# Optimization experiments

Measured on AMD Instinct MI355X. Metric: run time of the kernel, lower is better.

## Reference

```python
import jax, jax.numpy as jnp
import numpy as np

N = 10000; E = 160000; NF = 5; EF = 3; H = 8; C = 128; HC = H * C; G = 16

def _glorot(key, shape):
    s = float(np.sqrt(6.0 / (shape[0] + shape[-1])))
    return jax.random.uniform(key, shape, minval=-s, maxval=s, dtype=jnp.float32)

def setup_inputs():
    key = jax.random.key(0)
    ks = jax.random.split(key, 32)
    inp = {}
    inp["x"] = jax.random.normal(ks[0], (N, NF), dtype=jnp.float32)
    inp["edge_index"] = jax.random.randint(ks[1], (2, E), 0, N, dtype=jnp.int32)
    inp["edge_attr"] = jax.random.normal(ks[2], (E, EF), dtype=jnp.float32)
    inp["batch"] = jnp.sort(jax.random.randint(ks[3], (N,), 0, G, dtype=jnp.int32))
    ins = [NF, HC, HC, HC]
    i = 4
    for l in range(4):
        inp[f"W{l+1}"] = _glorot(ks[i], (ins[l], HC)); i += 1
        inp[f"We{l+1}"] = _glorot(ks[i], (EF, HC)); i += 1
        inp[f"as{l+1}"] = _glorot(ks[i], (H, C)); i += 1
        inp[f"ad{l+1}"] = _glorot(ks[i], (H, C)); i += 1
        inp[f"ae{l+1}"] = _glorot(ks[i], (H, C)); i += 1
        inp[f"b{l+1}"] = jnp.zeros((HC if l < 3 else C,), jnp.float32)
    inp["lin_w"] = _glorot(ks[i], (C, 1)) * 2.0
    inp["lin_b"] = jnp.zeros((1,), jnp.float32)
    return inp

def _gat(x, src, dst, ea, W, We, a_s, a_d, a_e, bias, concat):
    # PyG GATConv with edge_dim, add_self_loops=True, fill_value='mean'
    n = x.shape[0]
    cnt = jax.ops.segment_sum(jnp.ones((src.shape[0],), x.dtype), dst, n)
    loop_attr = jax.ops.segment_sum(ea, dst, n) / jnp.maximum(cnt, 1.0)[:, None]
    sl = jnp.arange(n, dtype=src.dtype)
    src2 = jnp.concatenate([src, sl])
    dst2 = jnp.concatenate([dst, sl])
    ea2 = jnp.concatenate([ea, loop_attr], axis=0)
    xl = (x @ W).reshape(n, H, C)                       # [N,H,C]
    a_src = jnp.einsum("nhc,hc->nh", xl, a_s)
    a_dst = jnp.einsum("nhc,hc->nh", xl, a_d)
    el = (ea2 @ We).reshape(-1, H, C)                    # [E2,H,C]
    alpha = a_src[src2] + a_dst[dst2] + jnp.einsum("ehc,hc->eh", el, a_e)
    alpha = jax.nn.leaky_relu(alpha, 0.2)
    m = jax.ops.segment_max(alpha, dst2, n)
    m = jnp.where(jnp.isfinite(m), m, 0.0)
    ex = jnp.exp(alpha - m[dst2])
    den = jax.ops.segment_sum(ex, dst2, n)
    alpha = ex / (den[dst2] + 1e-16)                     # segment softmax over dst
    out = jax.ops.segment_sum(alpha[:, :, None] * xl[src2], dst2, n)  # [N,H,C]
    if concat:
        return out.reshape(n, HC) + bias
    return out.mean(axis=1) + bias

def reference(x, edge_index, edge_attr, batch,
              W1, We1, as1, ad1, ae1, b1,
              W2, We2, as2, ad2, ae2, b2,
              W3, We3, as3, ad3, ae3, b3,
              W4, We4, as4, ad4, ae4, b4,
              lin_w, lin_b):
    src, dst = edge_index[0], edge_index[1]
    h = jax.nn.elu(_gat(x, src, dst, edge_attr, W1, We1, as1, ad1, ae1, b1, True))
    h = jax.nn.elu(_gat(h, src, dst, edge_attr, W2, We2, as2, ad2, ae2, b2, True))
    h = jax.nn.elu(_gat(h, src, dst, edge_attr, W3, We3, as3, ad3, ae3, b3, True))
    h = jax.nn.elu(_gat(h, src, dst, edge_attr, W4, We4, as4, ad4, ae4, b4, False))
    cnt = jax.ops.segment_sum(jnp.ones((N,), h.dtype), batch, G)
    pooled = jax.ops.segment_sum(h, batch, G) / jnp.maximum(cnt, 1.0)[:, None]
    return (pooled @ lin_w + lin_b).squeeze(-1)
```

## Files before the change

kernel.cpp:

```cpp
#include <hip/hip_runtime.h>
#include <math.h>

#define Nn 10000
#define En 160000
#define NF 5
#define EF 3
#define Hh 8
#define Cc 128
#define HC 1024
#define Gg 16

#define Mpad 10112

typedef __attribute__((ext_vector_type(8))) _Float16 half8;
typedef __attribute__((ext_vector_type(4))) float f32x4;


__device__ __forceinline__ void gl_lds16(const void* g, void* l) {
    __builtin_amdgcn_global_load_lds((const __attribute__((address_space(1))) void*)g,
                                     (__attribute__((address_space(3))) void*)l, 16, 0, 0);
}

__device__ __forceinline__ float elu_f(float v) {
    return (v > 0.f) ? v : expm1f(v);
}


__global__ void deg_sum_k(const int* __restrict__ dst, const float* __restrict__ ea,
                          int* __restrict__ cnt, float* __restrict__ sum_ea) {
    int e = blockIdx.x * 256 + threadIdx.x;
    if (e >= En) return;
    int d = dst[e];
    atomicAdd(&cnt[d], 1);
    atomicAdd(&sum_ea[d * 3 + 0], ea[e * 3 + 0]);
    atomicAdd(&sum_ea[d * 3 + 1], ea[e * 3 + 1]);
    atomicAdd(&sum_ea[d * 3 + 2], ea[e * 3 + 2]);
}

__global__ void finish_loop_k(const int* __restrict__ cnt, float* __restrict__ loop_attr) {
    int n = blockIdx.x * 256 + threadIdx.x;
    if (n >= Nn) return;
    float s = 1.0f / fmaxf((float)cnt[n], 1.0f);
    loop_attr[n * 3 + 0] *= s;
    loop_attr[n * 3 + 1] *= s;
    loop_attr[n * 3 + 2] *= s;
}

__global__ __launch_bounds__(1024) void scan_k(const int* __restrict__ cnt,
                                               int* __restrict__ rowptr,
                                               int* __restrict__ fillptr) {
    __shared__ int sh[1024];
    int tid = threadIdx.x;
    int base = 0;
    for (int chunk = 0; chunk < Nn; chunk += 1024) {
        int i = chunk + tid;
        int v = (i < Nn) ? cnt[i] : 0;
        sh[tid] = v;
        __syncthreads();
        for (int off = 1; off < 1024; off <<= 1) {
            int t = (tid >= off) ? sh[tid - off] : 0;
            __syncthreads();
            sh[tid] += t;
            __syncthreads();
        }
        int excl = sh[tid] - v;
        if (i < Nn) { rowptr[i] = base + excl; fillptr[i] = base + excl; }
        int total = sh[1023];
        __syncthreads();
        base += total;
    }
    if (tid == 0) rowptr[Nn] = base;
}

__global__ void csr_fill_k(const int* __restrict__ src, const int* __restrict__ dst,
                           const float* __restrict__ ea, int* __restrict__ fillptr,
                           int* __restrict__ srcP, float4* __restrict__ eaP) {
    int e = blockIdx.x * 256 + threadIdx.x;
    if (e >= En) return;
    int d = dst[e];
    int pos = atomicAdd(&fillptr[d], 1);
    srcP[pos] = src[e];
    eaP[pos] = make_float4(ea[e * 3 + 0], ea[e * 3 + 1], ea[e * 3 + 2], 0.f);
}

__global__ void bounds_k(const int* __restrict__ batch, int* __restrict__ gstart) {
    int i = blockIdx.x * 256 + threadIdx.x;
    if (i >= Nn) return;
    int b = batch[i];
    if (i == 0) {
        for (int g = 0; g <= b; ++g) gstart[g] = 0;
    } else {
        int pb = batch[i - 1];
        for (int g = pb + 1; g <= b; ++g) gstart[g] = i;
    }
    if (i == Nn - 1) {
        for (int g = b + 1; g <= Gg; ++g) gstart[g] = Nn;
    }
}


__global__ void wae_all_k(const float* __restrict__ We1, const float* __restrict__ ae1,
                          const float* __restrict__ We2, const float* __restrict__ ae2,
                          const float* __restrict__ We3, const float* __restrict__ ae3,
                          const float* __restrict__ We4, const float* __restrict__ ae4,
                          float* __restrict__ w_ae_all) {
    int t = threadIdx.x;
    if (t >= 96) return;
    int l = t / 24, idx = t % 24;
    int f = idx >> 3, h = idx & 7;
    const float* We = (l == 0) ? We1 : (l == 1) ? We2 : (l == 2) ? We3 : We4;
    const float* ae = (l == 0) ? ae1 : (l == 1) ? ae2 : (l == 2) ? ae3 : ae4;
    float s = 0.f;
    for (int c = 0; c < Cc; ++c) s += We[f * HC + h * Cc + c] * ae[h * Cc + c];
    w_ae_all[l * 24 + f * 8 + h] = s;
}

__global__ __launch_bounds__(1024) void wsplit_all_k(const float* __restrict__ W2,
                                                     const float* __restrict__ W3,
                                                     const float* __restrict__ W4,
                                                     _Float16* __restrict__ Wt16) {
    __shared__ float tile[32][33];
    int z = blockIdx.z;
    const float* W = (z == 0) ? W2 : (z == 1) ? W3 : W4;
    int nb = blockIdx.x * 32, kb = blockIdx.y * 32;
    tile[threadIdx.y][threadIdx.x] = W[(size_t)(kb + threadIdx.y) * HC + nb + threadIdx.x];
    __syncthreads();
    float x = tile[threadIdx.x][threadIdx.y];
    int n = nb + threadIdx.y, k = kb + threadIdx.x;
    Wt16[(size_t)z * HC * HC + (size_t)n * HC + k] = (_Float16)x;
}


__global__ void gemm_k5(const float* __restrict__ x, const float* __restrict__ Wm,
                        const float* __restrict__ a_s, const float* __restrict__ a_d,
                        _Float16* __restrict__ out16,
                        float* __restrict__ a_srcB, float* __restrict__ a_dstB) {
    int n = blockIdx.x;
    int tid = threadIdx.x;
    __shared__ float xr[8];
    __shared__ float vrow[HC];
    if (tid < NF) xr[tid] = x[n * NF + tid];
    __syncthreads();
    float x0 = xr[0], x1 = xr[1], x2 = xr[2], x3 = xr[3], x4 = xr[4];
    for (int j = tid; j < HC; j += 256) {
        float v = x0 * Wm[j] + x1 * Wm[HC + j] + x2 * Wm[2 * HC + j]
                + x3 * Wm[3 * HC + j] + x4 * Wm[4 * HC + j];
        out16[(size_t)n * HC + j] = (_Float16)v;
        vrow[j] = v;
    }
    __syncthreads();
    int w = tid >> 6, lane = tid & 63;
#pragma unroll
    for (int q = 0; q < 2; ++q) {
        int h = w * 2 + q;
        float v0 = vrow[h * Cc + lane], v1 = vrow[h * Cc + 64 + lane];
        float s1 = v0 * a_s[h * Cc + lane] + v1 * a_s[h * Cc + 64 + lane];
        float s2 = v0 * a_d[h * Cc + lane] + v1 * a_d[h * Cc + 64 + lane];
#pragma unroll
        for (int off = 32; off; off >>= 1) {
            s1 += __shfl_xor(s1, off);
            s2 += __shfl_xor(s2, off);
        }
        if (lane == 0) { a_srcB[n * 8 + h] = s1; a_dstB[n * 8 + h] = s2; }
    }
}

__global__ __launch_bounds__(256) void gemm_mfma(const _Float16* __restrict__ A,
                                                 const _Float16* __restrict__ Bt,
                                                 const float* __restrict__ a_s,
                                                 const float* __restrict__ a_d,
                                                 _Float16* __restrict__ C16,
                                                 float* __restrict__ a_srcB,
                                                 float* __restrict__ a_dstB) {
    __shared__ _Float16 As[128 * 32];
    __shared__ _Float16 Bs[128 * 32];
    __shared__ float ps[128][2];
    __shared__ float pd[128][2];
    int tid = threadIdx.x;
    int wave = tid >> 6, lane = tid & 63;
    int wr = wave >> 1, wc = wave & 1;
    int row0 = blockIdx.y * 128;
    int col0 = blockIdx.x * 128;
    int h = blockIdx.x;

    f32x4 acc[4][4];
#pragma unroll
    for (int i = 0; i < 4; ++i)
#pragma unroll
        for (int j = 0; j < 4; ++j) acc[i][j] = (f32x4){0.f, 0.f, 0.f, 0.f};

    int srow = lane >> 2;
    int scol = (lane & 3) * 8;
    int fr = lane & 15;
    int fk = (lane >> 4) * 8;

    for (int kb = 0; kb < 1024; kb += 32) {
#pragma unroll
        for (int cc = 0; cc < 2; ++cc) {
            int c = wave + cc * 4;
            int r = c * 16 + srow;
            gl_lds16(A + (size_t)(row0 + r) * 1024 + kb + scol, &As[c * 512 + lane * 8]);
            gl_lds16(Bt + (size_t)(col0 + r) * 1024 + kb + scol, &Bs[c * 512 + lane * 8]);
        }
        __syncthreads();

        half8 af[4], bf[4];
#pragma unroll
        for (int i = 0; i < 4; ++i)
            af[i] = *(const half8*)&As[(wr * 64 + i * 16 + fr) * 32 + fk];
#pragma unroll
        for (int j = 0; j < 4; ++j)
            bf[j] = *(const half8*)&Bs[(wc * 64 + j * 16 + fr) * 32 + fk];
#pragma unroll
        for (int i = 0; i < 4; ++i)
#pragma unroll
            for (int j = 0; j < 4; ++j)
                acc[i][j] = __builtin_amdgcn_mfma_f32_16x16x32_f16(af[i], bf[j], acc[i][j],
                                                                   0, 0, 0);
        __syncthreads();
    }

    int cn = lane & 15, rq = (lane >> 4) * 4;
#pragma unroll
    for (int i = 0; i < 4; ++i) {
        int rbase = row0 + wr * 64 + i * 16 + rq;
#pragma unroll
        for (int j = 0; j < 4; ++j) {
            int col = col0 + wc * 64 + j * 16 + cn;
#pragma unroll
            for (int r = 0; r < 4; ++r) {
                int row = rbase + r;
                if (row < Nn) C16[(size_t)row * HC + col] = (_Float16)acc[i][j][r];
            }
        }
    }
    float asv[4], adv[4];
#pragma unroll
    for (int j = 0; j < 4; ++j) {
        int c = wc * 64 + j * 16 + cn;
        asv[j] = a_s[h * Cc + c];
        adv[j] = a_d[h * Cc + c];
    }
#pragma unroll
    for (int i = 0; i < 4; ++i)
#pragma unroll
        for (int r = 0; r < 4; ++r) {
            float rs = acc[i][0][r] * asv[0] + acc[i][1][r] * asv[1]
                     + acc[i][2][r] * asv[2] + acc[i][3][r] * asv[3];
            float rd = acc[i][0][r] * adv[0] + acc[i][1][r] * adv[1]
                     + acc[i][2][r] * adv[2] + acc[i][3][r] * adv[3];
#pragma unroll
            for (int off = 1; off < 16; off <<= 1) {
                rs += __shfl_xor(rs, off);
                rd += __shfl_xor(rd, off);
            }
            if (cn == 0) {
                int rib = wr * 64 + i * 16 + rq + r;
                ps[rib][wc] = rs;
                pd[rib][wc] = rd;
            }
        }
    __syncthreads();
    if (tid < 128) {
        int row = row0 + tid;
        if (row < Nn) {
            a_srcB[row * 8 + h] = ps[tid][0] + ps[tid][1];
            a_dstB[row * 8 + h] = pd[tid][0] + pd[tid][1];
        }
    }
}


__global__ __launch_bounds__(256) void aggregate_k(const _Float16* __restrict__ xl16,
                                                   const float4* __restrict__ eaP,
                                                   const float* __restrict__ loop_attr,
                                                   const float* __restrict__ a_srcB,
                                                   const float* __restrict__ a_dstB,
                                                   const float* __restrict__ w_ae,
                                                   const int* __restrict__ rowptr,
                                                   const int* __restrict__ srcP,
                                                   const float* __restrict__ bias,
                                                   const float* __restrict__ lin_w,
                                                   _Float16* __restrict__ A2,
                                                   float* __restrict__ dnode,
                                                   int raw_mode) {
    int n = (blockIdx.x * 256 + threadIdx.x) >> 6;
    int lane = threadIdx.x & 63;
    if (n >= Nn) return;
    int beg = rowptr[n], end = rowptr[n + 1];
    int hh = lane & 7;
    int slot = lane >> 3;
    int hc = lane >> 3;

    float w0 = w_ae[hh], w1 = w_ae[8 + hh], w2 = w_ae[16 + hh];
    float adst_n = a_dstB[n * 8 + hh];
    float asrc_n = a_srcB[n * 8 + hh];
    float f0 = loop_attr[n * 3 + 0], f1 = loop_attr[n * 3 + 1], f2 = loop_attr[n * 3 + 2];
    float av = asrc_n + adst_n + f0 * w0 + f1 * w1 + f2 * w2;
    float aself = (av > 0.f) ? av : 0.2f * av;

    float m = (slot == 0) ? aself : -3.0e38f;
    float s = (slot == 0) ? 1.0f : 0.0f;
    for (int i = beg + slot; i < end; i += 8) {
        int sn = srcP[i];
        float4 e4 = eaP[i];
        float a = a_srcB[sn * 8 + hh] + adst_n + e4.x * w0 + e4.y * w1 + e4.z * w2;
        a = (a > 0.f) ? a : 0.2f * a;
        if (a > m) { s = s * __expf(m - a) + 1.0f; m = a; }
        else s += __expf(a - m);
    }
#pragma unroll
    for (int off = 8; off < 64; off <<= 1) {
        float mo = __shfl_xor(m, off);
        float so = __shfl_xor(s, off);
        float M = fmaxf(m, mo);
        s = s * __expf(m - M) + so * __expf(mo - M);
        m = M;
    }
    float inv = 1.f / (s + 1e-16f);
    float wself = __expf(aself - m) * inv;

    float m_c = __shfl(m, hc);
    float inv_c = __shfl(inv, hc);
    float wself_c = __shfl(wself, hc);
    float adst_nc = __shfl(adst_n, hc);
    float w0c = w_ae[hc], w1c = w_ae[8 + hc], w2c = w_ae[16 + hc];

    float acc[16];
    {
        const _Float16* r = xl16 + (size_t)n * HC + lane * 16;
        half8 r0 = *(const half8*)r;
        half8 r1 = *(const half8*)(r + 8);
#pragma unroll
        for (int j = 0; j < 8; ++j) {
            acc[j] = wself_c * (float)r0[j];
            acc[8 + j] = wself_c * (float)r1[j];
        }
    }
    int loff = lane * 16;
    for (int i0 = beg; i0 < end; i0 += 4) {
        int last = end - 1;
        bool v1 = (i0 + 1 < end), v2 = (i0 + 2 < end), v3 = (i0 + 3 < end);
        int i1 = v1 ? i0 + 1 : last;
        int i2 = v2 ? i0 + 2 : last;
        int i3 = v3 ? i0 + 3 : last;
        int s0 = srcP[i0], s1 = srcP[i1], s2 = srcP[i2], s3 = srcP[i3];
        float4 e0 = eaP[i0], e1 = eaP[i1], e2 = eaP[i2], e3 = eaP[i3];
        float as0 = a_srcB[s0 * 8 + hc], as1 = a_srcB[s1 * 8 + hc];
        float as2 = a_srcB[s2 * 8 + hc], as3 = a_srcB[s3 * 8 + hc];
        const _Float16* p0 = xl16 + (size_t)s0 * HC + loff;
        const _Float16* p1 = xl16 + (size_t)s1 * HC + loff;
        const _Float16* p2 = xl16 + (size_t)s2 * HC + loff;
        const _Float16* p3 = xl16 + (size_t)s3 * HC + loff;
        half8 q0a = *(const half8*)p0, q0b = *(const half8*)(p0 + 8);
        half8 q1a = *(const half8*)p1, q1b = *(const half8*)(p1 + 8);
        half8 q2a = *(const half8*)p2, q2b = *(const half8*)(p2 + 8);
        half8 q3a = *(const half8*)p3, q3b = *(const half8*)(p3 + 8);
        float al0 = as0 + adst_nc + e0.x * w0c + e0.y * w1c + e0.z * w2c;
        float al1 = as1 + adst_nc + e1.x * w0c + e1.y * w1c + e1.z * w2c;
        float al2 = as2 + adst_nc + e2.x * w0c + e2.y * w1c + e2.z * w2c;
        float al3 = as3 + adst_nc + e3.x * w0c + e3.y * w1c + e3.z * w2c;
        al0 = (al0 > 0.f) ? al0 : 0.2f * al0;
        al1 = v1 ? ((al1 > 0.f) ? al1 : 0.2f * al1) : -3.0e38f;
        al2 = v2 ? ((al2 > 0.f) ? al2 : 0.2f * al2) : -3.0e38f;
        al3 = v3 ? ((al3 > 0.f) ? al3 : 0.2f * al3) : -3.0e38f;
        float u0 = __expf(al0 - m_c) * inv_c;
        float u1 = __expf(al1 - m_c) * inv_c;
        float u2 = __expf(al2 - m_c) * inv_c;
        float u3 = __expf(al3 - m_c) * inv_c;
#pragma unroll
        for (int j = 0; j < 8; ++j) {
            float t0 = acc[j], t1 = acc[8 + j];
            t0 = fmaf(u0, (float)q0a[j], t0);  t1 = fmaf(u0, (float)q0b[j], t1);
            t0 = fmaf(u1, (float)q1a[j], t0);  t1 = fmaf(u1, (float)q1b[j], t1);
            t0 = fmaf(u2, (float)q2a[j], t0);  t1 = fmaf(u2, (float)q2b[j], t1);
            t0 = fmaf(u3, (float)q3a[j], t0);  t1 = fmaf(u3, (float)q3b[j], t1);
            acc[j] = t0; acc[8 + j] = t1;
        }
    }

    if (!raw_mode) {
        int ch = lane * 16;
        half8 hv0, hv1;
#pragma unroll
        for (int j = 0; j < 8; ++j) {
            hv0[j] = (_Float16)elu_f(acc[j] + bias[ch + j]);
            hv1[j] = (_Float16)elu_f(acc[8 + j] + bias[ch + 8 + j]);
        }
        _Float16* p = A2 + (size_t)n * 1024 + ch;
        *(half8*)p = hv0;
        *(half8*)(p + 8) = hv1;
    } else {
#pragma unroll
        for (int off = 8; off < 64; off <<= 1)
#pragma unroll
            for (int j = 0; j < 16; ++j) acc[j] += __shfl_xor(acc[j], off);
        int c0 = (lane & 7) * 16;
        float partial = 0.f;
#pragma unroll
        for (int j = 0; j < 16; ++j) {
            float v = elu_f(acc[j] * 0.125f + bias[c0 + j]);
            partial = fmaf(v, lin_w[c0 + j], partial);
        }
#pragma unroll
        for (int off = 1; off < 8; off <<= 1) partial += __shfl_xor(partial, off);
        if (lane == 0) dnode[n] = partial;
    }
}


__global__ __launch_bounds__(256) void pool_final_k(const float* __restrict__ dnode,
                                                    const int* __restrict__ gstart,
                                                    const float* __restrict__ lin_b,
                                                    float* __restrict__ out) {
    __shared__ float sh[256];
    int g = blockIdx.x;
    int tid = threadIdx.x;
    int s = gstart[g], e = gstart[g + 1];
    float acc = 0.f;
    for (int n = s + tid; n < e; n += 256) acc += dnode[n];
    sh[tid] = acc;
    __syncthreads();
    for (int off = 128; off; off >>= 1) {
        if (tid < off) sh[tid] += sh[tid + off];
        __syncthreads();
    }
    if (tid == 0) out[g] = sh[0] / fmaxf((float)(e - s), 1.f) + lin_b[0];
}


extern "C" void kernel_launch(void* const* d_in, const int* in_sizes, int n_in,
                              void* d_out, int out_size, void* d_ws, size_t ws_size,
                              hipStream_t stream) {
    const float* x = (const float*)d_in[0];
    const int* ei = (const int*)d_in[1];
    const float* ea = (const float*)d_in[2];
    const int* batch = (const int*)d_in[3];
    const float *Wl[4], *Wel[4], *asl[4], *adl[4], *ael[4], *bl[4];
    for (int l = 0; l < 4; ++l) {
        Wl[l] = (const float*)d_in[4 + 6 * l];
        Wel[l] = (const float*)d_in[5 + 6 * l];
        asl[l] = (const float*)d_in[6 + 6 * l];
        adl[l] = (const float*)d_in[7 + 6 * l];
        ael[l] = (const float*)d_in[8 + 6 * l];
        bl[l] = (const float*)d_in[9 + 6 * l];
    }
    const float* lin_w = (const float*)d_in[28];
    const float* lin_b = (const float*)d_in[29];
    const int* srcA = ei;
    const int* dstA = ei + En;

    float* Wp = (float*)d_ws;
    size_t o = 0;
    _Float16* A2 = (_Float16*)(Wp + o); o += (size_t)Mpad * 512;
    _Float16* Wt16 = (_Float16*)(Wp + o); o += (size_t)3 * HC * HC / 2;
    _Float16* xl16 = (_Float16*)(Wp + o); o += (size_t)Nn * HC / 2;
    float4* eaP = (float4*)(Wp + o); o += (size_t)En * 4;
    float* loop_attr = Wp + o; o += Nn * 3;
    int* cnt = (int*)(Wp + o); o += Nn;
    int* rowptr = (int*)(Wp + o); o += Nn + 1;
    int* fillptr = (int*)(Wp + o); o += Nn;
    int* srcP = (int*)(Wp + o); o += En;
    int* gstart = (int*)(Wp + o); o += Gg + 1;
    float* a_srcB = Wp + o; o += Nn * Hh;
    float* a_dstB = Wp + o; o += Nn * Hh;
    float* w_ae_all = Wp + o; o += 128;
    float* dnode = Wp + o; o += Nn;

    hipMemsetAsync(cnt, 0, Nn * sizeof(int), stream);
    hipMemsetAsync(loop_attr, 0, Nn * 3 * sizeof(float), stream);

    deg_sum_k<<<(En + 255) / 256, 256, 0, stream>>>(dstA, ea, cnt, loop_attr);
    finish_loop_k<<<(Nn + 255) / 256, 256, 0, stream>>>(cnt, loop_attr);
    scan_k<<<1, 1024, 0, stream>>>(cnt, rowptr, fillptr);
    csr_fill_k<<<(En + 255) / 256, 256, 0, stream>>>(srcA, dstA, ea, fillptr, srcP, eaP);
    bounds_k<<<(Nn + 255) / 256, 256, 0, stream>>>(batch, gstart);
    wae_all_k<<<1, 128, 0, stream>>>(Wel[0], ael[0], Wel[1], ael[1], Wel[2], ael[2],
                                     Wel[3], ael[3], w_ae_all);
    wsplit_all_k<<<dim3(32, 32, 3), dim3(32, 32), 0, stream>>>(Wl[1], Wl[2], Wl[3], Wt16);

    for (int l = 0; l < 4; ++l) {
        if (l == 0)
            gemm_k5<<<Nn, 256, 0, stream>>>(x, Wl[0], asl[0], adl[0], xl16, a_srcB, a_dstB);
        else
            gemm_mfma<<<dim3(HC / 128, Mpad / 128), 256, 0, stream>>>(
                A2, Wt16 + (size_t)(l - 1) * HC * HC, asl[l], adl[l], xl16, a_srcB, a_dstB);
        aggregate_k<<<(Nn + 3) / 4, 256, 0, stream>>>(xl16, eaP, loop_attr, a_srcB,
                                                      a_dstB, w_ae_all + l * 24, rowptr,
                                                      srcP, bl[l], lin_w, A2, dnode,
                                                      (l == 3) ? 1 : 0);
    }
    pool_final_k<<<Gg, 256, 0, stream>>>(dnode, gstart, lin_b, (float*)d_out);
}
```

Measured before the change: 599.0 us.

## Split each node's edge aggregation across two waves and fold loop-attr normalize into scan

The aggregation kernel now gives each destination node two wavefronts that take alternating groups of edges. Their fp32 partial sums are combined through shared memory before the ELU/bias epilogue or the final-layer reduction. This raises parallelism and memory-level concurrency for the gather-bound loop, at the cost of a block barrier, an LDS round trip and duplicated softmax statistic computation. The separate loop-attribute normalization kernel is merged into the prefix-scan kernel to save one launch.

Result: no change. 603.1 us (+0.7%).

```diff
diff --git a/kernel.cpp b/kernel.cpp
--- a/kernel.cpp
+++ b/kernel.cpp
@@ -37,24 +37,22 @@
     atomicAdd(&sum_ea[d * 3 + 2], ea[e * 3 + 2]);
 }
 
-__global__ void finish_loop_k(const int* __restrict__ cnt, float* __restrict__ loop_attr) {
-    int n = blockIdx.x * 256 + threadIdx.x;
-    if (n >= Nn) return;
-    float s = 1.0f / fmaxf((float)cnt[n], 1.0f);
-    loop_attr[n * 3 + 0] *= s;
-    loop_attr[n * 3 + 1] *= s;
-    loop_attr[n * 3 + 2] *= s;
-}
-
 __global__ __launch_bounds__(1024) void scan_k(const int* __restrict__ cnt,
                                                int* __restrict__ rowptr,
-                                               int* __restrict__ fillptr) {
+                                               int* __restrict__ fillptr,
+                                               float* __restrict__ loop_attr) {
     __shared__ int sh[1024];
     int tid = threadIdx.x;
     int base = 0;
     for (int chunk = 0; chunk < Nn; chunk += 1024) {
         int i = chunk + tid;
         int v = (i < Nn) ? cnt[i] : 0;
+        if (i < Nn) {
+            float s = 1.0f / fmaxf((float)v, 1.0f);
+            loop_attr[i * 3 + 0] *= s;
+            loop_attr[i * 3 + 1] *= s;
+            loop_attr[i * 3 + 2] *= s;
+        }
         sh[tid] = v;
         __syncthreads();
         for (int off = 1; off < 1024; off <<= 1) {
@@ -284,9 +282,12 @@
                                                    _Float16* __restrict__ A2,
                                                    float* __restrict__ dnode,
                                                    int raw_mode) {
-    int n = (blockIdx.x * 256 + threadIdx.x) >> 6;
+    __shared__ float cmb[2][1024];
+    int wave = threadIdx.x >> 6;
     int lane = threadIdx.x & 63;
-    if (n >= Nn) return;
+    int nl = wave >> 1;
+    int sub = wave & 1;
+    int n = blockIdx.x * 2 + nl;
     int beg = rowptr[n], end = rowptr[n + 1];
     int hh = lane & 7;
     int slot = lane >> 3;
@@ -327,7 +328,7 @@
     float w0c = w_ae[hc], w1c = w_ae[8 + hc], w2c = w_ae[16 + hc];
 
     float acc[16];
-    {
+    if (sub == 0) {
         const _Float16* r = xl16 + (size_t)n * HC + lane * 16;
         half8 r0 = *(const half8*)r;
         half8 r1 = *(const half8*)(r + 8);
@@ -336,14 +337,17 @@
             acc[j] = wself_c * (float)r0[j];
             acc[8 + j] = wself_c * (float)r1[j];
         }
+    } else {
+#pragma unroll
+        for (int j = 0; j < 16; ++j) acc[j] = 0.f;
     }
     int loff = lane * 16;
-    for (int i0 = beg; i0 < end; i0 += 4) {
-        int last = end - 1;
-        bool v1 = (i0 + 1 < end), v2 = (i0 + 2 < end), v3 = (i0 + 3 < end);
-        int i1 = v1 ? i0 + 1 : last;
-        int i2 = v2 ? i0 + 2 : last;
-        int i3 = v3 ? i0 + 3 : last;
+    for (int i0 = beg + sub; i0 < end; i0 += 8) {
+        int i1 = i0 + 2, i2 = i0 + 4, i3 = i0 + 6;
+        bool v1 = (i1 < end), v2 = (i2 < end), v3 = (i3 < end);
+        if (!v1) i1 = i0;
+        if (!v2) i2 = i0;
+        if (!v3) i3 = i0;
         int s0 = srcP[i0], s1 = srcP[i1], s2 = srcP[i2], s3 = srcP[i3];
         float4 e0 = eaP[i0], e1 = eaP[i1], e2 = eaP[i2], e3 = eaP[i3];
         float as0 = a_srcB[s0 * 8 + hc], as1 = a_srcB[s1 * 8 + hc];
@@ -379,32 +383,48 @@
         }
     }
 
-    if (!raw_mode) {
-        int ch = lane * 16;
-        half8 hv0, hv1;
-#pragma unroll
-        for (int j = 0; j < 8; ++j) {
-            hv0[j] = (_Float16)elu_f(acc[j] + bias[ch + j]);
-            hv1[j] = (_Float16)elu_f(acc[8 + j] + bias[ch + 8 + j]);
-        }
-        _Float16* p = A2 + (size_t)n * 1024 + ch;
-        *(half8*)p = hv0;
-        *(half8*)(p + 8) = hv1;
-    } else {
-#pragma unroll
-        for (int off = 8; off < 64; off <<= 1)
-#pragma unroll
-            for (int j = 0; j < 16; ++j) acc[j] += __shfl_xor(acc[j], off);
-        int c0 = (lane & 7) * 16;
-        float partial = 0.f;
-#pragma unroll
-        for (int j = 0; j < 16; ++j) {
-            float v = elu_f(acc[j] * 0.125f + bias[c0 + j]);
-            partial = fmaf(v, lin_w[c0 + j], partial);
-        }
-#pragma unroll
-        for (int off = 1; off < 8; off <<= 1) partial += __shfl_xor(partial, off);
-        if (lane == 0) dnode[n] = partial;
+    if (sub == 0) {
+#pragma unroll
+        for (int j = 0; j < 4; ++j)
+            *(float4*)&cmb[nl][loff + j * 4] = *(float4*)&acc[j * 4];
+    }
+    __syncthreads();
+    if (sub == 1) {
+#pragma unroll
+        for (int j = 0; j < 4; ++j) {
+            float4 c4 = *(const float4*)&cmb[nl][loff + j * 4];
+            acc[j * 4 + 0] += c4.x;
+            acc[j * 4 + 1] += c4.y;
+            acc[j * 4 + 2] += c4.z;
+            acc[j * 4 + 3] += c4.w;
+        }
+        if (!raw_mode) {
+            int ch = loff;
+            half8 hv0, hv1;
+#pragma unroll
+            for (int j = 0; j < 8; ++j) {
+                hv0[j] = (_Float16)elu_f(acc[j] + bias[ch + j]);
+                hv1[j] = (_Float16)elu_f(acc[8 + j] + bias[ch + 8 + j]);
+            }
+            _Float16* p = A2 + (size_t)n * 1024 + ch;
+            *(half8*)p = hv0;
+            *(half8*)(p + 8) = hv1;
+        } else {
+#pragma unroll
+            for (int off = 8; off < 64; off <<= 1)
+#pragma unroll
+                for (int j = 0; j < 16; ++j) acc[j] += __shfl_xor(acc[j], off);
+            int c0 = (lane & 7) * 16;
+            float partial = 0.f;
+#pragma unroll
+            for (int j = 0; j < 16; ++j) {
+                float v = elu_f(acc[j] * 0.125f + bias[c0 + j]);
+                partial = fmaf(v, lin_w[c0 + j], partial);
+            }
+#pragma unroll
+            for (int off = 1; off < 8; off <<= 1) partial += __shfl_xor(partial, off);
+            if (lane == 0) dnode[n] = partial;
+        }
     }
 }
 
@@ -471,8 +491,7 @@
     hipMemsetAsync(loop_attr, 0, Nn * 3 * sizeof(float), stream);
 
     deg_sum_k<<<(En + 255) / 256, 256, 0, stream>>>(dstA, ea, cnt, loop_attr);
-    finish_loop_k<<<(Nn + 255) / 256, 256, 0, stream>>>(cnt, loop_attr);
-    scan_k<<<1, 1024, 0, stream>>>(cnt, rowptr, fillptr);
+    scan_k<<<1, 1024, 0, stream>>>(cnt, rowptr, fillptr, loop_attr);
     csr_fill_k<<<(En + 255) / 256, 256, 0, stream>>>(srcA, dstA, ea, fillptr, srcP, eaP);
     bounds_k<<<(Nn + 255) / 256, 256, 0, stream>>>(batch, gstart);
     wae_all_k<<<1, 128, 0, stream>>>(Wel[0], ael[0], Wel[1], ael[1], Wel[2], ael[2],
@@ -485,10 +504,10 @@
         else
             gemm_mfma<<<dim3(HC / 128, Mpad / 128), 256, 0, stream>>>(
                 A2, Wt16 + (size_t)(l - 1) * HC * HC, asl[l], adl[l], xl16, a_srcB, a_dstB);
-        aggregate_k<<<(Nn + 3) / 4, 256, 0, stream>>>(xl16, eaP, loop_attr, a_srcB,
-                                                      a_dstB, w_ae_all + l * 24, rowptr,
-                                                      srcP, bl[l], lin_w, A2, dnode,
-                                                      (l == 3) ? 1 : 0);
+        aggregate_k<<<Nn / 2, 256, 0, stream>>>(xl16, eaP, loop_attr, a_srcB,
+                                                a_dstB, w_ae_all + l * 24, rowptr,
+                                                srcP, bl[l], lin_w, A2, dnode,
+                                                (l == 3) ? 1 : 0);
     }
     pool_final_k<<<Gg, 256, 0, stream>>>(dnode, gstart, lin_b, (float*)d_out);
 }
```
